# Performance work log

Measured on AMD Instinct MI355X. Metric: run time of the kernel, lower is better.

The kernel has to match this reference:

```python
import jax, jax.numpy as jnp
import numpy as np

# Fixed supermask = [3, 4, 16, 28, 0, 0, 0, 3]:
#   preproc: relu(Linear x3); l1 = GCN(x); l2 = GCN(l1); l3 = GCN(l2);
#   out = relu(Linear z3((l1+l2+l3)/3))
HIDDEN = 64


def gcn_conv(h, W, b, src, dst, norm, n_nodes):
    # PyG GCNConv: h' = scatter_add(norm * (hW)[src] -> dst) + b
    hw = h @ W                                  # [N, F]
    msg = hw[src] * norm[:, None]               # gather + scale  [E+N, F]
    agg = jax.ops.segment_sum(msg, dst, num_segments=n_nodes)
    return agg + b


def setup_inputs() -> dict:
    key = jax.random.key(0)
    ks = jax.random.split(key, 12)
    N, E, NFEAT, NCLASS = 100000, 1000000, 256, 40
    x = jax.random.normal(ks[0], (N, NFEAT), dtype=jnp.float32)
    edge_index = jax.random.randint(ks[1], (2, E), 0, N, dtype=jnp.int64)
    s = 1.0 / np.sqrt(NFEAT)
    h = 1.0 / np.sqrt(HIDDEN)
    return {
        "x": x,
        "edge_index": edge_index,
        "Wx": jax.random.uniform(ks[2], (NFEAT, HIDDEN), jnp.float32, -s, s),
        "bx": jnp.zeros((HIDDEN,), jnp.float32),
        "W1": jax.random.uniform(ks[3], (HIDDEN, HIDDEN), jnp.float32, -h, h),
        "b1": jnp.zeros((HIDDEN,), jnp.float32),
        "W2": jax.random.uniform(ks[4], (HIDDEN, HIDDEN), jnp.float32, -h, h),
        "b2": jnp.zeros((HIDDEN,), jnp.float32),
        "W3": jax.random.uniform(ks[5], (HIDDEN, HIDDEN), jnp.float32, -h, h),
        "b3": jnp.zeros((HIDDEN,), jnp.float32),
        "Wz": jax.random.uniform(ks[6], (HIDDEN, NCLASS), jnp.float32, -h, h),
        "bz": jnp.zeros((NCLASS,), jnp.float32),
    }


def reference(x, edge_index, Wx, bx, W1, b1, W2, b2, W3, b3, Wz, bz):
    n = x.shape[0]
    # add self-loops (PyG GCNConv default)
    loop = jnp.arange(n, dtype=edge_index.dtype)
    src = jnp.concatenate([edge_index[0], loop])
    dst = jnp.concatenate([edge_index[1], loop])
    deg = jax.ops.segment_sum(jnp.ones_like(dst, dtype=x.dtype), dst, num_segments=n)
    dinv = jnp.where(deg > 0, jax.lax.rsqrt(deg), 0.0)
    norm = dinv[src] * dinv[dst]                 # [E+N]

    h0 = jax.nn.relu(x @ Wx + bx)                # x_3(relu) o x3(Linear)
    l1 = gcn_conv(h0, W1, b1, src, dst, norm, n)
    l2 = gcn_conv(l1, W2, b2, src, dst, norm, n)
    l3 = gcn_conv(l2, W3, b3, src, dst, norm, n)
    z = (l1 + l2 + l3) / 3.0
    return jax.nn.relu(z @ Wz + bz)
```

## Files before the change

kernel.cpp:

```cpp
#include <hip/hip_runtime.h>

#define NFEAT 256
#define HID 64
#define NCLASS 40
#define EPB 4096
#define BCAP 8192

typedef _Float16 half8 __attribute__((ext_vector_type(8)));
typedef float floatx4 __attribute__((ext_vector_type(4)));

__device__ __forceinline__ int wave_iscan(int v, int lane) {
    #pragma unroll
    for (int o = 1; o < 64; o <<= 1) {
        int u = __shfl_up(v, o, 64);
        if (lane >= o) v += u;
    }
    return v;
}

template<int NT>
__device__ __forceinline__ int block_iscan(int v, int t, int* wsum) {
    const int NW = NT / 64;
    int lane = t & 63, wv = t >> 6;
    int s = wave_iscan(v, lane);
    if (lane == 63) wsum[wv] = s;
    __syncthreads();
    if (wv == 0) {
        int w = (lane < NW) ? wsum[lane] : 0;
        #pragma unroll
        for (int o = 1; o < NW; o <<= 1) {
            int u = __shfl_up(w, o, 64);
            if (lane >= o) w += u;
        }
        if (lane < NW) wsum[lane] = w;
    }
    __syncthreads();
    int add = (wv > 0) ? wsum[wv - 1] : 0;
    return s + add;
}

struct BinSM {
    int lcnt[256], loff[256], lcur[256], gbase[256], wsum[4];
    int sdst[EPB];
    int words[EPB];
};

__global__ __launch_bounds__(256) void k_pre(const int* __restrict__ src, const int* __restrict__ dst,
                                             int* __restrict__ bcur, int* __restrict__ bwords,
                                             int nbuckets, int E, int nbin,
                                             const float* __restrict__ W1, const float* __restrict__ W2,
                                             const float* __restrict__ W3, _Float16* __restrict__ Wt16,
                                             const float* __restrict__ x, const float* __restrict__ Wx,
                                             const float* __restrict__ bx, _Float16* __restrict__ h0,
                                             int N, int ngemm) {
    __shared__ __align__(16) char smraw[sizeof(BinSM)];
    int t = threadIdx.x;
    int bid = blockIdx.x;

    if (bid >= nbin && bid < nbin + 3) {
        int l = bid - nbin;
        const float* Ws = (l == 0) ? W1 : (l == 1) ? W2 : W3;
        _Float16* wt = Wt16 + l * 4096;
        for (int i = t; i < 4096; i += 256) {
            int col = i >> 6, k = i & 63;
            wt[i] = (_Float16)Ws[k * HID + col];
        }
        return;
    }

    if (bid >= nbin + 3) {
        _Float16 (*Wt)[264] = (_Float16 (*)[264])smraw;
        {
            int c = t & 63, k0 = (t >> 6) * 64;
            for (int k = k0; k < k0 + 64; ++k)
                Wt[c][k] = (_Float16)Wx[k * HID + c];
        }
        __syncthreads();
        int lane = t & 63, wv = t >> 6;
        int lg = lane >> 4, ln = lane & 15;
        int gb = bid - nbin - 3;
        int wid = gb * 4 + wv;
        int nw = ngemm * 4;
        float bb[4];
        #pragma unroll
        for (int g = 0; g < 4; ++g) bb[g] = bx[g * 16 + ln];
        int ntiles = N >> 4;
        for (int tile = wid; tile < ntiles; tile += nw) {
            int row0 = tile << 4;
            const float* xr = x + (size_t)(row0 + ln) * NFEAT + lg * 8;
            float4 av[16];
            #pragma unroll
            for (int ks = 0; ks < 8; ++ks) {
                av[2 * ks]     = *(const float4*)(xr + ks * 32);
                av[2 * ks + 1] = *(const float4*)(xr + ks * 32 + 4);
            }
            floatx4 acc[4] = {{0.f,0.f,0.f,0.f},{0.f,0.f,0.f,0.f},{0.f,0.f,0.f,0.f},{0.f,0.f,0.f,0.f}};
            #pragma unroll
            for (int ks = 0; ks < 8; ++ks) {
                float4 a0 = av[2 * ks], a1 = av[2 * ks + 1];
                half8 a;
                a[0]=(_Float16)a0.x; a[1]=(_Float16)a0.y; a[2]=(_Float16)a0.z; a[3]=(_Float16)a0.w;
                a[4]=(_Float16)a1.x; a[5]=(_Float16)a1.y; a[6]=(_Float16)a1.z; a[7]=(_Float16)a1.w;
                #pragma unroll
                for (int g = 0; g < 4; ++g) {
                    half8 b = *(const half8*)&Wt[g * 16 + ln][ks * 32 + lg * 8];
                    acc[g] = __builtin_amdgcn_mfma_f32_16x16x32_f16(a, b, acc[g], 0, 0, 0);
                }
            }
            #pragma unroll
            for (int g = 0; g < 4; ++g) {
                #pragma unroll
                for (int r = 0; r < 4; ++r) {
                    int row = row0 + lg * 4 + r;
                    h0[(size_t)row * HID + g * 16 + ln] = (_Float16)fmaxf(acc[g][r] + bb[g], 0.f);
                }
            }
        }
        return;
    }

    BinSM* sm = (BinSM*)smraw;
    int base = bid * EPB;
    int n = E - base; if (n > EPB) n = EPB;
    sm->lcnt[t] = 0;
    __syncthreads();
    for (int i = t; i < n; i += 256) {
        int d = dst[base + i];
        sm->sdst[i] = d;
        atomicAdd(&sm->lcnt[d >> 9], 1);
    }
    __syncthreads();
    int v = sm->lcnt[t];
    int incl = block_iscan<256>(v, t, sm->wsum);
    int excl = incl - v;
    sm->loff[t] = excl; sm->lcur[t] = excl;
    __syncthreads();
    for (int i = t; i < n; i += 256) {
        int d = sm->sdst[i], s = src[base + i];
        int b = d >> 9;
        int p = atomicAdd(&sm->lcur[b], 1);
        sm->words[p] = s | ((d & 511) << 17);
    }
    __syncthreads();
    if (t < nbuckets) {
        int c = sm->lcnt[t];
        sm->gbase[t] = c > 0 ? atomicAdd(&bcur[t], c) : 0;
    }
    __syncthreads();
    int lane = t & 63, wv = t >> 6;
    for (int b = wv; b < nbuckets; b += 4) {
        int o = sm->loff[b], c = sm->lcnt[b], gb = sm->gbase[b];
        int* dstp = bwords + (size_t)b * BCAP;
        for (int i = lane; i < c; i += 64) {
            int gp = gb + i;
            if (gp < BCAP) dstp[gp] = sm->words[o + i];
        }
    }
}

__global__ __launch_bounds__(256) void k_csr(const int* __restrict__ bcur, const int* __restrict__ bwords,
                                             int* __restrict__ csr, unsigned* __restrict__ pk,
                                             float* __restrict__ dinv, int* __restrict__ order, int N) {
    __shared__ int cnt[512], cur[512], wsum[4];
    __shared__ int hist[32], hcur[32];
    __shared__ int lcsr[BCAP];
    int t = threadIdx.x;
    int b = blockIdx.x;
    int nodebase = b << 9;
    int nb = bcur[b]; if (nb > BCAP) nb = BCAP;
    cnt[t] = 0; cnt[t + 256] = 0;
    if (t < 32) hist[t] = 0;
    __syncthreads();
    const int* wp = bwords + (size_t)b * BCAP;
    for (int i = t; i < nb; i += 256)
        atomicAdd(&cnt[wp[i] >> 17], 1);
    __syncthreads();
    int v0 = cnt[2 * t], v1 = cnt[2 * t + 1];
    int p = v0 + v1;
    int incl = block_iscan<256>(p, t, wsum);
    int e = incl - p;
    cur[2 * t] = e; cur[2 * t + 1] = e + v0;
    int kc0 = (v0 + 7) >> 3; if (kc0 > 31) kc0 = 31;
    int kc1 = (v1 + 7) >> 3; if (kc1 > 31) kc1 = 31;
    atomicAdd(&hist[kc0], 1);
    atomicAdd(&hist[kc1], 1);
    #pragma unroll
    for (int j = 0; j < 2; ++j) {
        int node = nodebase + 2 * t + j;
        if (node < N) {
            int c = cnt[2 * t + j]; if (c > 2047) c = 2047;
            pk[node] = (unsigned)(b * BCAP + cur[2 * t + j]) | ((unsigned)c << 21);
            dinv[node] = rsqrtf((float)c + 1.0f);
        }
    }
    __syncthreads();
    if (t < 32) {
        int h = hist[t];
        int s = h;
        #pragma unroll
        for (int o = 1; o < 32; o <<= 1) {
            int u = __shfl_up(s, o, 32);
            if ((t & 31) >= o) s += u;
        }
        hcur[t] = s - h;
    }
    __syncthreads();
    {
        int r0 = atomicAdd(&hcur[kc0], 1);
        int r1 = atomicAdd(&hcur[kc1], 1);
        order[(b << 9) + r0] = nodebase + 2 * t;
        order[(b << 9) + r1] = nodebase + 2 * t + 1;
    }
    for (int i = t; i < nb; i += 256) {
        int w = wp[i];
        int pos = atomicAdd(&cur[w >> 17], 1);
        lcsr[pos] = w & 0x1FFFF;
    }
    __syncthreads();
    int* cp = csr + (size_t)b * BCAP;
    for (int i = t; i < nb; i += 256) cp[i] = lcsr[i];
}

template<int WRN, int FUSE>
__global__ __launch_bounds__(256) void k_layer(const _Float16* __restrict__ Ph, const int* __restrict__ csr,
                                               const unsigned* __restrict__ pk, const float* __restrict__ dinv,
                                               const _Float16* __restrict__ Wt, const float* __restrict__ b,
                                               float* __restrict__ normf, const int* __restrict__ order,
                                               _Float16* __restrict__ Lout, int N,
                                               const _Float16* __restrict__ L1p, const _Float16* __restrict__ L2p,
                                               const float* __restrict__ Wz, const float* __restrict__ bz,
                                               float* __restrict__ outp) {
    __shared__ _Float16 z[32][72];
    __shared__ _Float16 ot[32][72];
    __shared__ float oout[32][48];
    int t = threadIdx.x;
    int lane = t & 63, wv = t >> 6;
    int sg = lane >> 3, f8 = lane & 7;
    int lg = lane >> 4, ln = lane & 15;
    int nb = blockIdx.x << 5;
    int node = order[nb + wv * 8 + sg];
    bool valid = node < N;
    int nodec = valid ? node : 0;
    int col = wv * 16 + ln;
    half8 bf0 = *(const half8*)(Wt + col * 64 + lg * 8);
    half8 bf1 = *(const half8*)(Wt + col * 64 + 32 + lg * 8);
    float bb = b[col];

    unsigned pkv = valid ? pk[node] : 0u;
    int off = (int)(pkv & 0x1FFFFFu);
    int c = valid ? (int)(pkv >> 21) : 0;
    float dd = valid ? dinv[node] : 0.f;
    const _Float16* pb = Ph + f8 * 8;
    float acc[8];
    {
        half8 self = *(const half8*)(pb + (size_t)nodec * HID);
        float dd2 = dd * dd;
        #pragma unroll
        for (int j = 0; j < 8; ++j) acc[j] = (float)self[j] * dd2;
    }
    int ecur = f8;
    bool ok = ecur < c;
    int s_cur = ok ? csr[off + ecur] : nodec;
    float nm_cur;
    if (WRN) {
        nm_cur = ok ? dinv[s_cur] * dd : 0.f;
        if (ok) normf[off + ecur] = nm_cur;
    } else {
        nm_cur = ok ? normf[off + ecur] : 0.f;
    }
    for (int jj = 0; jj < c; jj += 8) {
        int en = jj + 8 + f8;
        bool okn = en < c;
        int s_nxt = okn ? csr[off + en] : nodec;
        float nm_nxt;
        if (WRN) {
            nm_nxt = okn ? dinv[s_nxt] * dd : 0.f;
            if (okn) normf[off + en] = nm_nxt;
        } else {
            nm_nxt = okn ? normf[off + en] : 0.f;
        }
        #pragma unroll
        for (int j = 0; j < 8; ++j) {
            int ss = __shfl(s_cur, j, 8);
            float nn = __shfl(nm_cur, j, 8);
            half8 v = *(const half8*)(pb + (size_t)ss * HID);
            #pragma unroll
            for (int q = 0; q < 8; ++q) acc[q] = fmaf((float)v[q], nn, acc[q]);
        }
        s_cur = s_nxt; nm_cur = nm_nxt;
    }
    {
        half8 zv;
        #pragma unroll
        for (int j = 0; j < 8; ++j) zv[j] = (_Float16)acc[j];
        *(half8*)&z[wv * 8 + sg][f8 * 8] = zv;
    }
    __syncthreads();
    floatx4 acc0 = {0.f, 0.f, 0.f, 0.f}, acc1 = {0.f, 0.f, 0.f, 0.f};
    {
        half8 a0 = *(const half8*)&z[ln][lg * 8];
        half8 a1 = *(const half8*)&z[16 + ln][lg * 8];
        acc0 = __builtin_amdgcn_mfma_f32_16x16x32_f16(a0, bf0, acc0, 0, 0, 0);
        acc1 = __builtin_amdgcn_mfma_f32_16x16x32_f16(a1, bf0, acc1, 0, 0, 0);
        a0 = *(const half8*)&z[ln][32 + lg * 8];
        a1 = *(const half8*)&z[16 + ln][32 + lg * 8];
        acc0 = __builtin_amdgcn_mfma_f32_16x16x32_f16(a0, bf1, acc0, 0, 0, 0);
        acc1 = __builtin_amdgcn_mfma_f32_16x16x32_f16(a1, bf1, acc1, 0, 0, 0);
    }
    #pragma unroll
    for (int r = 0; r < 4; ++r) {
        ot[lg * 4 + r][wv * 16 + ln] = (_Float16)(acc0[r] + bb);
        ot[16 + lg * 4 + r][wv * 16 + ln] = (_Float16)(acc1[r] + bb);
    }
    __syncthreads();

    if (!FUSE) {
        int row = t >> 3, c8 = t & 7;
        int onode = order[nb + row];
        if (onode < N)
            *(half8*)(Lout + (size_t)onode * HID + c8 * 8) = *(const half8*)&ot[row][c8 * 8];
    } else {
        {
            int row = t >> 3, c8 = t & 7;
            int onode = order[nb + row];
            half8 a1, a2;
            if (onode < N) {
                a1 = *(const half8*)(L1p + (size_t)onode * HID + c8 * 8);
                a2 = *(const half8*)(L2p + (size_t)onode * HID + c8 * 8);
            } else {
                #pragma unroll
                for (int j = 0; j < 8; ++j) { a1[j] = (_Float16)0.f; a2[j] = (_Float16)0.f; }
            }
            half8 l3 = *(const half8*)&ot[row][c8 * 8];
            half8 s;
            #pragma unroll
            for (int j = 0; j < 8; ++j)
                s[j] = (_Float16)(((float)a1[j] + (float)a2[j] + (float)l3[j]) * (1.f / 3.f));
            *(half8*)&z[row][c8 * 8] = s;
        }
        __syncthreads();
        for (int tk = wv; tk < 6; tk += 4) {
            int rt = tk / 3, cg = tk % 3;
            int ocol = cg * 16 + ln;
            bool okc = ocol < NCLASS;
            half8 bw0, bw1;
            #pragma unroll
            for (int j = 0; j < 8; ++j) {
                bw0[j] = okc ? (_Float16)Wz[(lg * 8 + j) * NCLASS + ocol] : (_Float16)0.f;
                bw1[j] = okc ? (_Float16)Wz[(32 + lg * 8 + j) * NCLASS + ocol] : (_Float16)0.f;
            }
            float bbz = okc ? bz[ocol] : 0.f;
            floatx4 ac = {0.f, 0.f, 0.f, 0.f};
            half8 a0 = *(const half8*)&z[rt * 16 + ln][lg * 8];
            ac = __builtin_amdgcn_mfma_f32_16x16x32_f16(a0, bw0, ac, 0, 0, 0);
            a0 = *(const half8*)&z[rt * 16 + ln][32 + lg * 8];
            ac = __builtin_amdgcn_mfma_f32_16x16x32_f16(a0, bw1, ac, 0, 0, 0);
            #pragma unroll
            for (int r = 0; r < 4; ++r)
                oout[rt * 16 + lg * 4 + r][cg * 16 + ln] = fmaxf(ac[r] + bbz, 0.f);
        }
        __syncthreads();
        for (int i = t; i < 32 * NCLASS; i += 256) {
            int row = i / NCLASS, ocol = i % NCLASS;
            int onode = order[nb + row];
            if (onode < N)
                outp[(size_t)onode * NCLASS + ocol] = oout[row][ocol];
        }
    }
}

extern "C" void kernel_launch(void* const* d_in, const int* in_sizes, int n_in,
                              void* d_out, int out_size, void* d_ws, size_t ws_size,
                              hipStream_t stream) {
    const float* x  = (const float*)d_in[0];
    const int*   ei = (const int*)d_in[1];
    const float* Wx = (const float*)d_in[2];
    const float* bx = (const float*)d_in[3];
    const float* W1 = (const float*)d_in[4];
    const float* b1 = (const float*)d_in[5];
    const float* W2 = (const float*)d_in[6];
    const float* b2 = (const float*)d_in[7];
    const float* W3 = (const float*)d_in[8];
    const float* b3 = (const float*)d_in[9];
    const float* Wz = (const float*)d_in[10];
    const float* bz = (const float*)d_in[11];
    float* out = (float*)d_out;

    int N = in_sizes[0] / NFEAT;
    int E = in_sizes[1] / 2;
    const int* src = ei;
    const int* dst = ei + E;
    int nbuckets = (N + 511) >> 9;

    size_t nh = (size_t)N * HID;
    size_t Npad = ((size_t)N + 7) / 8 * 8;
    int*      bcur = (int*)d_ws;
    float*    dinv = (float*)d_ws + 256;
    unsigned* pk   = (unsigned*)(dinv + Npad);
    _Float16* H0   = (_Float16*)(pk + Npad);
    _Float16* L1   = H0 + nh;
    _Float16* L2   = L1 + nh;
    _Float16* L3   = L2 + nh;
    int*      bwords = (int*)(L3 + nh);
    int*      csr  = bwords + (size_t)nbuckets * BCAP;
    _Float16* Wt16 = (_Float16*)(csr + (size_t)nbuckets * BCAP);
    float*    normf = (float*)(Wt16 + 3 * 4096);
    int*      order = (int*)(normf + (size_t)nbuckets * BCAP);

    int nbin = (E + EPB - 1) / EPB;
    int ngemm = 512;
    hipMemsetAsync(bcur, 0, 256 * sizeof(int), stream);
    k_pre<<<nbin + 3 + ngemm, 256, 0, stream>>>(src, dst, bcur, bwords, nbuckets, E, nbin,
                                                W1, W2, W3, Wt16, x, Wx, bx, H0, N, ngemm);
    k_csr<<<nbuckets, 256, 0, stream>>>(bcur, bwords, csr, pk, dinv, order, N);

    int layer_blocks = nbuckets * 16;
    k_layer<1,0><<<layer_blocks, 256, 0, stream>>>(H0, csr, pk, dinv, Wt16,        b1, normf, order, L1, N,
                                                   nullptr, nullptr, nullptr, nullptr, nullptr);
    k_layer<0,0><<<layer_blocks, 256, 0, stream>>>(L1, csr, pk, dinv, Wt16 + 4096, b2, normf, order, L2, N,
                                                   nullptr, nullptr, nullptr, nullptr, nullptr);
    k_layer<0,1><<<layer_blocks, 256, 0, stream>>>(L2, csr, pk, dinv, Wt16 + 8192, b3, normf, order, L3, N,
                                                   L1, L2, Wz, bz, out);
}
```

Measured before the change: 314.7 us.

## Drop degree-sorted node order and double-buffer neighbor row gathers

Removes the per-bucket degree histogram and order permutation from the CSR build, so layer kernels process nodes in natural index order with fewer blocks. The edge aggregation loop now keeps two register buffers of eight gathered neighbor rows, issuing the next batch's loads before accumulating the current one to hide gather latency. This trades degree-balanced waves for more memory-level parallelism and higher register pressure, and imbalanced degrees within a wave may cause divergence.

```diff
diff --git a/kernel.cpp b/kernel.cpp
--- a/kernel.cpp
+++ b/kernel.cpp
@@ -160,16 +160,14 @@
 
 __global__ __launch_bounds__(256) void k_csr(const int* __restrict__ bcur, const int* __restrict__ bwords,
                                              int* __restrict__ csr, unsigned* __restrict__ pk,
-                                             float* __restrict__ dinv, int* __restrict__ order, int N) {
+                                             float* __restrict__ dinv, int N) {
     __shared__ int cnt[512], cur[512], wsum[4];
-    __shared__ int hist[32], hcur[32];
     __shared__ int lcsr[BCAP];
     int t = threadIdx.x;
     int b = blockIdx.x;
     int nodebase = b << 9;
     int nb = bcur[b]; if (nb > BCAP) nb = BCAP;
     cnt[t] = 0; cnt[t + 256] = 0;
-    if (t < 32) hist[t] = 0;
     __syncthreads();
     const int* wp = bwords + (size_t)b * BCAP;
     for (int i = t; i < nb; i += 256)
@@ -180,10 +178,6 @@
     int incl = block_iscan<256>(p, t, wsum);
     int e = incl - p;
     cur[2 * t] = e; cur[2 * t + 1] = e + v0;
-    int kc0 = (v0 + 7) >> 3; if (kc0 > 31) kc0 = 31;
-    int kc1 = (v1 + 7) >> 3; if (kc1 > 31) kc1 = 31;
-    atomicAdd(&hist[kc0], 1);
-    atomicAdd(&hist[kc1], 1);
     #pragma unroll
     for (int j = 0; j < 2; ++j) {
         int node = nodebase + 2 * t + j;
@@ -194,23 +188,6 @@
         }
     }
     __syncthreads();
-    if (t < 32) {
-        int h = hist[t];
-        int s = h;
-        #pragma unroll
-        for (int o = 1; o < 32; o <<= 1) {
-            int u = __shfl_up(s, o, 32);
-            if ((t & 31) >= o) s += u;
-        }
-        hcur[t] = s - h;
-    }
-    __syncthreads();
-    {
-        int r0 = atomicAdd(&hcur[kc0], 1);
-        int r1 = atomicAdd(&hcur[kc1], 1);
-        order[(b << 9) + r0] = nodebase + 2 * t;
-        order[(b << 9) + r1] = nodebase + 2 * t + 1;
-    }
     for (int i = t; i < nb; i += 256) {
         int w = wp[i];
         int pos = atomicAdd(&cur[w >> 17], 1);
@@ -225,22 +202,22 @@
 __global__ __launch_bounds__(256) void k_layer(const _Float16* __restrict__ Ph, const int* __restrict__ csr,
                                                const unsigned* __restrict__ pk, const float* __restrict__ dinv,
                                                const _Float16* __restrict__ Wt, const float* __restrict__ b,
-                                               float* __restrict__ normf, const int* __restrict__ order,
+                                               float* __restrict__ normf,
                                                _Float16* __restrict__ Lout, int N,
                                                const _Float16* __restrict__ L1p, const _Float16* __restrict__ L2p,
                                                const float* __restrict__ Wz, const float* __restrict__ bz,
                                                float* __restrict__ outp) {
     __shared__ _Float16 z[32][72];
     __shared__ _Float16 ot[32][72];
-    __shared__ float oout[32][48];
+    __shared__ float oout[FUSE ? 32 : 1][FUSE ? 48 : 1];
     int t = threadIdx.x;
     int lane = t & 63, wv = t >> 6;
     int sg = lane >> 3, f8 = lane & 7;
     int lg = lane >> 4, ln = lane & 15;
     int nb = blockIdx.x << 5;
-    int node = order[nb + wv * 8 + sg];
+    int node = nb + wv * 8 + sg;
     bool valid = node < N;
-    int nodec = valid ? node : 0;
+    int nodec = valid ? node : (N - 1);
     int col = wv * 16 + ln;
     half8 bf0 = *(const half8*)(Wt + col * 64 + lg * 8);
     half8 bf1 = *(const half8*)(Wt + col * 64 + 32 + lg * 8);
@@ -258,36 +235,66 @@
         #pragma unroll
         for (int j = 0; j < 8; ++j) acc[j] = (float)self[j] * dd2;
     }
-    int ecur = f8;
-    bool ok = ecur < c;
-    int s_cur = ok ? csr[off + ecur] : nodec;
-    float nm_cur;
+    half8 RA[8], RB[8];
+    int eA0 = f8, eB0 = 8 + f8;
+    bool okA = eA0 < c, okB = eB0 < c;
+    int sA = okA ? csr[off + eA0] : nodec;
+    int sB = okB ? csr[off + eB0] : nodec;
+    float nmA, nmB;
     if (WRN) {
-        nm_cur = ok ? dinv[s_cur] * dd : 0.f;
-        if (ok) normf[off + ecur] = nm_cur;
+        nmA = okA ? dinv[sA] * dd : 0.f; if (okA) normf[off + eA0] = nmA;
+        nmB = okB ? dinv[sB] * dd : 0.f; if (okB) normf[off + eB0] = nmB;
     } else {
-        nm_cur = ok ? normf[off + ecur] : 0.f;
-    }
-    for (int jj = 0; jj < c; jj += 8) {
-        int en = jj + 8 + f8;
-        bool okn = en < c;
-        int s_nxt = okn ? csr[off + en] : nodec;
-        float nm_nxt;
-        if (WRN) {
-            nm_nxt = okn ? dinv[s_nxt] * dd : 0.f;
-            if (okn) normf[off + en] = nm_nxt;
-        } else {
-            nm_nxt = okn ? normf[off + en] : 0.f;
-        }
+        nmA = okA ? normf[off + eA0] : 0.f;
+        nmB = okB ? normf[off + eB0] : 0.f;
+    }
+    #pragma unroll
+    for (int j = 0; j < 8; ++j) {
+        int ss = __shfl(sA, j, 8);
+        RA[j] = *(const half8*)(pb + (size_t)ss * HID);
+    }
+    for (int jj = 0; jj < c; jj += 16) {
         #pragma unroll
         for (int j = 0; j < 8; ++j) {
-            int ss = __shfl(s_cur, j, 8);
-            float nn = __shfl(nm_cur, j, 8);
-            half8 v = *(const half8*)(pb + (size_t)ss * HID);
-            #pragma unroll
-            for (int q = 0; q < 8; ++q) acc[q] = fmaf((float)v[q], nn, acc[q]);
-        }
-        s_cur = s_nxt; nm_cur = nm_nxt;
+            int ss = __shfl(sB, j, 8);
+            RB[j] = *(const half8*)(pb + (size_t)ss * HID);
+        }
+        {
+            int e2 = jj + 16 + f8;
+            bool ok2 = e2 < c;
+            int s2 = ok2 ? csr[off + e2] : nodec;
+            float nm2;
+            if (WRN) { nm2 = ok2 ? dinv[s2] * dd : 0.f; if (ok2) normf[off + e2] = nm2; }
+            else nm2 = ok2 ? normf[off + e2] : 0.f;
+            #pragma unroll
+            for (int j = 0; j < 8; ++j) {
+                float nn = __shfl(nmA, j, 8);
+                #pragma unroll
+                for (int q = 0; q < 8; ++q) acc[q] = fmaf((float)RA[j][q], nn, acc[q]);
+            }
+            sA = s2; nmA = nm2;
+        }
+        if (jj + 8 >= c) break;
+        #pragma unroll
+        for (int j = 0; j < 8; ++j) {
+            int ss = __shfl(sA, j, 8);
+            RA[j] = *(const half8*)(pb + (size_t)ss * HID);
+        }
+        {
+            int e2 = jj + 24 + f8;
+            bool ok2 = e2 < c;
+            int s2 = ok2 ? csr[off + e2] : nodec;
+            float nm2;
+            if (WRN) { nm2 = ok2 ? dinv[s2] * dd : 0.f; if (ok2) normf[off + e2] = nm2; }
+            else nm2 = ok2 ? normf[off + e2] : 0.f;
+            #pragma unroll
+            for (int j = 0; j < 8; ++j) {
+                float nn = __shfl(nmB, j, 8);
+                #pragma unroll
+                for (int q = 0; q < 8; ++q) acc[q] = fmaf((float)RB[j][q], nn, acc[q]);
+            }
+            sB = s2; nmB = nm2;
+        }
     }
     {
         half8 zv;
@@ -316,13 +323,13 @@
 
     if (!FUSE) {
         int row = t >> 3, c8 = t & 7;
-        int onode = order[nb + row];
+        int onode = nb + row;
         if (onode < N)
             *(half8*)(Lout + (size_t)onode * HID + c8 * 8) = *(const half8*)&ot[row][c8 * 8];
     } else {
         {
             int row = t >> 3, c8 = t & 7;
-            int onode = order[nb + row];
+            int onode = nb + row;
             half8 a1, a2;
             if (onode < N) {
                 a1 = *(const half8*)(L1p + (size_t)onode * HID + c8 * 8);
@@ -362,7 +369,7 @@
         __syncthreads();
         for (int i = t; i < 32 * NCLASS; i += 256) {
             int row = i / NCLASS, ocol = i % NCLASS;
-            int onode = order[nb + row];
+            int onode = nb + row;
             if (onode < N)
                 outp[(size_t)onode * NCLASS + ocol] = oout[row][ocol];
         }
@@ -405,20 +412,19 @@
     int*      csr  = bwords + (size_t)nbuckets * BCAP;
     _Float16* Wt16 = (_Float16*)(csr + (size_t)nbuckets * BCAP);
     float*    normf = (float*)(Wt16 + 3 * 4096);
-    int*      order = (int*)(normf + (size_t)nbuckets * BCAP);
 
     int nbin = (E + EPB - 1) / EPB;
     int ngemm = 512;
     hipMemsetAsync(bcur, 0, 256 * sizeof(int), stream);
     k_pre<<<nbin + 3 + ngemm, 256, 0, stream>>>(src, dst, bcur, bwords, nbuckets, E, nbin,
                                                 W1, W2, W3, Wt16, x, Wx, bx, H0, N, ngemm);
-    k_csr<<<nbuckets, 256, 0, stream>>>(bcur, bwords, csr, pk, dinv, order, N);
-
-    int layer_blocks = nbuckets * 16;
-    k_layer<1,0><<<layer_blocks, 256, 0, stream>>>(H0, csr, pk, dinv, Wt16,        b1, normf, order, L1, N,
+    k_csr<<<nbuckets, 256, 0, stream>>>(bcur, bwords, csr, pk, dinv, N);
+
+    int layer_blocks = (N + 31) / 32;
+    k_layer<1,0><<<layer_blocks, 256, 0, stream>>>(H0, csr, pk, dinv, Wt16,        b1, normf, L1, N,
                                                    nullptr, nullptr, nullptr, nullptr, nullptr);
-    k_layer<0,0><<<layer_blocks, 256, 0, stream>>>(L1, csr, pk, dinv, Wt16 + 4096, b2, normf, order, L2, N,
+    k_layer<0,0><<<layer_blocks, 256, 0, stream>>>(L1, csr, pk, dinv, Wt16 + 4096, b2, normf, L2, N,
                                                    nullptr, nullptr, nullptr, nullptr, nullptr);
-    k_layer<0,1><<<layer_blocks, 256, 0, stream>>>(L2, csr, pk, dinv, Wt16 + 8192, b3, normf, order, L3, N,
+    k_layer<0,1><<<layer_blocks, 256, 0, stream>>>(L2, csr, pk, dinv, Wt16 + 8192, b3, normf, L3, N,
                                                    L1, L2, Wz, bz, out);
 }
```

Result: slower. 322.3 us (+2.4%).
